# Kernel tuning notes

Hardware: AMD Instinct MI355X
Metric: run time of the kernel (lower is better)

The kernel has to match this reference:

```python
import jax, jax.numpy as jnp
import numpy as np

LMAX = 2
C = 128            # uniform multiplicity per degree
H = 128            # hidden channels
M = (LMAX + 1) ** 2  # 9 spherical coefficients
EPS = 1e-6


def _pack_indices():
    # flat layout per degree block: [mul, 2l+1] channel-major; packed layout: [coeff, channel]
    pack = np.zeros(M * C, dtype=np.int64)
    offset = 0
    for l in range(LMAX + 1):
        dim = 2 * l + 1
        for m in range(dim):
            coeff = l * l + m
            for c in range(C):
                pack[coeff * C + c] = offset + c * dim + m
        offset += C * dim
    unpack = np.argsort(pack)
    return jnp.asarray(pack), jnp.asarray(unpack)

PACK_IDX, UNPACK_IDX = _pack_indices()
# expand_index: degree index for each of the M coefficients
EXPAND_IDX = jnp.asarray(np.repeat(np.arange(LMAX + 1), 2 * np.arange(LMAX + 1) + 1))


def setup_inputs() -> dict:
    key = jax.random.key(0)
    ks = jax.random.split(key, 6)
    N = 10000
    A = 42  # (2*(lmax+1)) * (2*(lmax+1)+1) = 6*7 flattened S2 grid points
    bound = 1.0 / np.sqrt(C)
    return {
        "x": jax.random.normal(ks[0], (N, M * C), dtype=jnp.float32),
        "norm_weight": jnp.ones((LMAX + 1, C), dtype=jnp.float32),
        "w1": jax.random.uniform(ks[1], (LMAX + 1, H, C), jnp.float32, -bound, bound),
        "b1": jnp.zeros((1, 1, H), dtype=jnp.float32),
        "grid_w": jax.random.uniform(ks[2], (2 * H, H), jnp.float32, -bound, bound),
        "grid_b": jnp.zeros((2 * H,), dtype=jnp.float32),
        "w2": jax.random.uniform(ks[3], (LMAX + 1, C, H), jnp.float32, -bound, bound),
        "b2": jnp.zeros((1, 1, C), dtype=jnp.float32),
        "to_grid_mat": jax.random.normal(ks[4], (A, M), dtype=jnp.float32) * 0.3,
        "from_grid_mat": jax.random.normal(ks[5], (M, A), dtype=jnp.float32) * 0.3,
    }


def reference(x, norm_weight, w1, b1, grid_w, grid_b, w2, b2, to_grid_mat, from_grid_mat):
    N = x.shape[0]
    # --- pack flat irreps -> [N, M, C] (pure permutation gather; no padding for uniform irreps)
    p = jnp.take(x, PACK_IDX, axis=1).reshape(N, M, C)
    # --- merged equivariant RMS norm over all (coeff, channel), per-degree-channel affine
    rms = jnp.sqrt(jnp.mean(p * p, axis=(1, 2), keepdims=True) + EPS)
    h = (p / rms) * norm_weight[EXPAND_IDX][None]  # [N, M, C]
    # --- SO3LinearFlat #1: per-degree dense C -> H, bias only on l=0 coeff
    h = jnp.einsum("nmc,mhc->nmh", h, w1[EXPAND_IDX])
    h = h.at[:, 0:1, :].add(b1)
    # --- to S2 grid: [N, M, H] -> [N, A, H]
    g = jnp.einsum("am,nmh->nah", to_grid_mat, h)
    # --- pointwise SwiGLU on grid: H -> 2H linear, silu gate
    z = jnp.einsum("nah,oh->nao", g, grid_w) + grid_b
    g = jax.nn.silu(z[..., :H]) * z[..., H:]
    # --- from S2 grid: [N, A, H] -> [N, M, H]
    h = jnp.einsum("ma,nah->nmh", from_grid_mat, g)
    # --- SO3LinearFlat #2: per-degree dense H -> C, bias only on l=0 coeff
    out = jnp.einsum("nmh,mch->nmc", h, w2[EXPAND_IDX])
    out = out.at[:, 0:1, :].add(b2)
    # --- unpack back to flat irreps layout
    return jnp.take(out.reshape(N, M * C), UNPACK_IDX, axis=1)
```

## Files before the change

kernel.cpp:

```cpp
#include <hip/hip_runtime.h>
#include <math.h>

typedef unsigned short u16;
typedef __attribute__((ext_vector_type(8))) short bf16x8;
typedef __attribute__((ext_vector_type(4))) float f32x4;
typedef __attribute__((ext_vector_type(16))) float f32x16;

constexpr int OFF_W1 = 0;
constexpr int OFF_W2 = 49152;
constexpr int OFF_GW = 98304;
constexpr int OFF_TG = 131072;
constexpr int OFF_FG = 132096;
constexpr int WS_ELEMS = 134144;

__device__ __forceinline__ u16 f2bf(float f) {
    unsigned u = __float_as_uint(f);
    u += 0x7FFFu + ((u >> 16) & 1u);
    return (u16)(u >> 16);
}

__global__ void prep_kernel(const float* __restrict__ w1, const float* __restrict__ gw,
                            const float* __restrict__ w2, const float* __restrict__ tg,
                            const float* __restrict__ fg, u16* __restrict__ wsb) {
    const int idx = blockIdx.x * blockDim.x + threadIdx.x;
    const int str = gridDim.x * blockDim.x;
    for (int i = idx; i < 49152; i += str) wsb[OFF_W1 + i] = f2bf(w1[i]);
    for (int i = idx; i < 49152; i += str) wsb[OFF_W2 + i] = f2bf(w2[i]);
    for (int i = idx; i < 32768; i += str) wsb[OFF_GW + i] = f2bf(gw[i]);
    for (int i = idx; i < 1024; i += str) {
        int a = i >> 4, k = i & 15;
        wsb[OFF_TG + i] = (a < 42 && k < 9) ? f2bf(tg[a * 9 + k]) : (u16)0;
    }
    for (int i = idx; i < 2048; i += str) {
        int m = i >> 6, k = i & 63;
        wsb[OFF_FG + i] = (m < 9 && k < 42) ? f2bf(fg[m * 42 + k]) : (u16)0;
    }
}

__global__ __launch_bounds__(256, 2) void eqffn_mfma(
    const float* __restrict__ x, const float* __restrict__ nw,
    const float* __restrict__ b1f, const float* __restrict__ gbf,
    const float* __restrict__ b2f, const u16* __restrict__ wsb,
    float* __restrict__ out, int N)
{
    __shared__ u16 sh_a1[64 * 136];
    __shared__ u16 sh_h1T[4 * 128 * 16];
    __shared__ u16 sh_g[48 * 136];
    __shared__ u16 sh_g2T[128 * 72];
    __shared__ float sh_nw[384];
    __shared__ float sh_b1[128];
    __shared__ float sh_b2[128];
    __shared__ float sh_gb[256];

    const int tid  = threadIdx.x;
    const int w    = tid >> 6;
    const int lane = tid & 63;
    const int q    = lane >> 4;
    const int r    = lane & 15;
    const int r32  = lane & 31;
    const int half = lane >> 5;
    const int n0   = blockIdx.x * 4;

    for (int i = tid; i < 384; i += 256) sh_nw[i] = nw[i];
    if (tid < 128) { sh_b1[tid] = b1f[tid]; sh_b2[tid] = b2f[tid]; }
    sh_gb[tid] = gbf[tid];
    {
        unsigned long long* z1 = (unsigned long long*)sh_h1T;
        for (int i = tid; i < 2048; i += 256) z1[i] = 0ull;
        unsigned long long* z2 = (unsigned long long*)sh_g2T;
        for (int i = tid; i < 2304; i += 256) z2[i] = 0ull;
    }
    __syncthreads();

    const int myn = n0 + w;
    float4 xv[5];
    float ss = 0.f;
    if (myn < N) {
        const float4* xr = (const float4*)(x + (size_t)myn * 1152);
        for (int i = lane, c2 = 0; i < 288; i += 64, ++c2) {
            float4 v = xr[i]; xv[c2] = v;
            ss += v.x * v.x + v.y * v.y + v.z * v.z + v.w * v.w;
        }
    }
    #pragma unroll
    for (int off = 32; off; off >>= 1) ss += __shfl_xor(ss, off);
    const float inv = 1.0f / sqrtf(ss * (1.0f / 1152.0f) + 1e-6f);
    if (myn < N) {
        for (int i = lane, c2 = 0; i < 288; i += 64, ++c2) {
            float4 v = xv[c2];
            #pragma unroll
            for (int e = 0; e < 4; ++e) {
                const int f = i * 4 + e;
                const float val = ((const float*)&v)[e] * inv;
                int row, c, l;
                if (f < 128)      { l = 0; c = f;            row = w; }
                else if (f < 512) { int t = f - 128; l = 1; c = t / 3; row = 16 + w * 3 + (t - c * 3); }
                else              { int t = f - 512; l = 2; c = t / 5; row = 32 + w * 5 + (t - c * 5); }
                sh_a1[row * 136 + c] = f2bf(val * sh_nw[l * 128 + c]);
            }
        }
    }
    __syncthreads();

    {
        f32x4 acc[4][2];
        #pragma unroll
        for (int a = 0; a < 4; ++a)
            #pragma unroll
            for (int b = 0; b < 2; ++b)
                #pragma unroll
                for (int e = 0; e < 4; ++e) acc[a][b][e] = 0.f;
        #pragma unroll
        for (int mt = 0; mt < 4; ++mt) {
            const int l = (mt == 0) ? 0 : ((mt == 1) ? 1 : 2);
            #pragma unroll
            for (int k = 0; k < 4; ++k) {
                bf16x8 af = *(const bf16x8*)&sh_a1[(mt * 16 + r) * 136 + k * 32 + q * 8];
                #pragma unroll
                for (int nt = 0; nt < 2; ++nt) {
                    const int h = (2 * w + nt) * 16 + r;
                    bf16x8 bf = *(const bf16x8*)&wsb[OFF_W1 + (l * 128 + h) * 128 + k * 32 + q * 8];
                    acc[mt][nt] = __builtin_amdgcn_mfma_f32_16x16x32_bf16(af, bf, acc[mt][nt], 0, 0, 0);
                }
            }
        }
        #pragma unroll
        for (int mt = 0; mt < 4; ++mt) {
            #pragma unroll
            for (int nt = 0; nt < 2; ++nt) {
                const int h = (2 * w + nt) * 16 + r;
                #pragma unroll
                for (int rg = 0; rg < 4; ++rg) {
                    const int rr = q * 4 + rg;
                    const float v = acc[mt][nt][rg];
                    if (mt == 0) {
                        if (rr < 4) sh_h1T[(rr * 128 + h) * 16 + 0] = f2bf(v + sh_b1[h]);
                    } else if (mt == 1) {
                        if (rr < 12) { int nd = rr / 3, mm = rr - nd * 3; sh_h1T[(nd * 128 + h) * 16 + 1 + mm] = f2bf(v); }
                    } else {
                        int rr2 = (mt - 2) * 16 + rr;
                        if (rr2 < 20) { int nd = rr2 / 5, mm = rr2 - nd * 5; sh_h1T[(nd * 128 + h) * 16 + 4 + mm] = f2bf(v); }
                    }
                }
            }
        }
    }
    __syncthreads();

    for (int nn = 0; nn < 4; ++nn) {
        {
            bf16x8 bfr = *(const bf16x8*)&sh_h1T[(nn * 128 + w * 32 + r32) * 16 + half * 8];
            bf16x8 a0  = *(const bf16x8*)&wsb[OFF_TG + r32 * 16 + half * 8];
            bf16x8 a1  = *(const bf16x8*)&wsb[OFF_TG + (32 + r32) * 16 + half * 8];
            f32x16 ac0, ac1;
            #pragma unroll
            for (int e = 0; e < 16; ++e) { ac0[e] = 0.f; ac1[e] = 0.f; }
            ac0 = __builtin_amdgcn_mfma_f32_32x32x16_bf16(a0, bfr, ac0, 0, 0, 0);
            ac1 = __builtin_amdgcn_mfma_f32_32x32x16_bf16(a1, bfr, ac1, 0, 0, 0);
            const int h = w * 32 + r32;
            #pragma unroll
            for (int rg = 0; rg < 16; ++rg) {
                const int ar = (rg & 3) + 8 * (rg >> 2) + 4 * half;
                sh_g[ar * 136 + h] = f2bf(ac0[rg]);
                const int ar1 = 32 + ar;
                if (ar1 < 48) sh_g[ar1 * 136 + h] = f2bf(ac1[rg]);
            }
        }
        __syncthreads();

        {
            bf16x8 bfr[3][4];
            #pragma unroll
            for (int nt = 0; nt < 3; ++nt)
                #pragma unroll
                for (int k = 0; k < 4; ++k)
                    bfr[nt][k] = *(const bf16x8*)&sh_g[(nt * 16 + r) * 136 + k * 32 + q * 8];
            f32x4 aL[2][3], aH[2][3];
            #pragma unroll
            for (int p = 0; p < 2; ++p)
                #pragma unroll
                for (int nt = 0; nt < 3; ++nt)
                    #pragma unroll
                    for (int e = 0; e < 4; ++e) { aL[p][nt][e] = 0.f; aH[p][nt][e] = 0.f; }
            #pragma unroll
            for (int p = 0; p < 2; ++p) {
                const int oL = (2 * w + p) * 16 + r;
                const int oH = oL + 128;
                #pragma unroll
                for (int k = 0; k < 4; ++k) {
                    bf16x8 fL = *(const bf16x8*)&wsb[OFF_GW + oL * 128 + k * 32 + q * 8];
                    bf16x8 fH = *(const bf16x8*)&wsb[OFF_GW + oH * 128 + k * 32 + q * 8];
                    #pragma unroll
                    for (int nt = 0; nt < 3; ++nt) {
                        aL[p][nt] = __builtin_amdgcn_mfma_f32_16x16x32_bf16(fL, bfr[nt][k], aL[p][nt], 0, 0, 0);
                        aH[p][nt] = __builtin_amdgcn_mfma_f32_16x16x32_bf16(fH, bfr[nt][k], aH[p][nt], 0, 0, 0);
                    }
                }
            }
            #pragma unroll
            for (int p = 0; p < 2; ++p) {
                #pragma unroll
                for (int nt = 0; nt < 3; ++nt) {
                    #pragma unroll
                    for (int rg = 0; rg < 4; ++rg) {
                        const int o = (2 * w + p) * 16 + q * 4 + rg;
                        const int a = nt * 16 + r;
                        const float zl = aL[p][nt][rg] + sh_gb[o];
                        const float zh = aH[p][nt][rg] + sh_gb[128 + o];
                        const float gv = zl * (1.0f / (1.0f + __expf(-zl))) * zh;
                        if (a < 42) sh_g2T[o * 72 + a] = f2bf(gv);
                    }
                }
            }
        }
        __syncthreads();

        {
            f32x16 ac;
            #pragma unroll
            for (int e = 0; e < 16; ++e) ac[e] = 0.f;
            const int h = w * 32 + r32;
            #pragma unroll
            for (int k = 0; k < 4; ++k) {
                bf16x8 af = *(const bf16x8*)&wsb[OFF_FG + r32 * 64 + k * 16 + half * 8];
                bf16x8 bf = *(const bf16x8*)&sh_g2T[h * 72 + k * 16 + half * 8];
                ac = __builtin_amdgcn_mfma_f32_32x32x16_bf16(af, bf, ac, 0, 0, 0);
            }
            #pragma unroll
            for (int rg = 0; rg < 16; ++rg) {
                const int m = (rg & 3) + 8 * (rg >> 2) + 4 * half;
                if (m < 9) {
                    const int row = (m == 0) ? nn : ((m < 4) ? (16 + nn * 3 + (m - 1)) : (32 + nn * 5 + (m - 4)));
                    sh_a1[row * 136 + h] = f2bf(ac[rg]);
                }
            }
        }
    }
    __syncthreads();

    {
        f32x4 acc[4][2];
        #pragma unroll
        for (int a = 0; a < 4; ++a)
            #pragma unroll
            for (int b = 0; b < 2; ++b)
                #pragma unroll
                for (int e = 0; e < 4; ++e) acc[a][b][e] = 0.f;
        #pragma unroll
        for (int mt = 0; mt < 4; ++mt) {
            const int l = (mt == 0) ? 0 : ((mt == 1) ? 1 : 2);
            #pragma unroll
            for (int k = 0; k < 4; ++k) {
                bf16x8 af = *(const bf16x8*)&sh_a1[(mt * 16 + r) * 136 + k * 32 + q * 8];
                #pragma unroll
                for (int nt = 0; nt < 2; ++nt) {
                    const int c = (2 * w + nt) * 16 + r;
                    bf16x8 bf = *(const bf16x8*)&wsb[OFF_W2 + (l * 128 + c) * 128 + k * 32 + q * 8];
                    acc[mt][nt] = __builtin_amdgcn_mfma_f32_16x16x32_bf16(af, bf, acc[mt][nt], 0, 0, 0);
                }
            }
        }
        #pragma unroll
        for (int mt = 0; mt < 4; ++mt) {
            #pragma unroll
            for (int nt = 0; nt < 2; ++nt) {
                const int c = (2 * w + nt) * 16 + r;
                #pragma unroll
                for (int rg = 0; rg < 4; ++rg) {
                    const int rr = q * 4 + rg;
                    const float v = acc[mt][nt][rg];
                    if (mt == 0) {
                        if (rr < 4) { int gn = n0 + rr; if (gn < N) out[(size_t)gn * 1152 + c] = v + sh_b2[c]; }
                    } else if (mt == 1) {
                        if (rr < 12) { int nd = rr / 3, mm = rr - nd * 3; int gn = n0 + nd;
                                       if (gn < N) out[(size_t)gn * 1152 + 128 + c * 3 + mm] = v; }
                    } else {
                        int rr2 = (mt - 2) * 16 + rr;
                        if (rr2 < 20) { int nd = rr2 / 5, mm = rr2 - nd * 5; int gn = n0 + nd;
                                        if (gn < N) out[(size_t)gn * 1152 + 512 + c * 5 + mm] = v; }
                    }
                }
            }
        }
    }
}

extern "C" void kernel_launch(void* const* d_in, const int* in_sizes, int n_in,
                              void* d_out, int out_size, void* d_ws, size_t ws_size,
                              hipStream_t stream)
{
    const float* x  = (const float*)d_in[0];
    const float* nw = (const float*)d_in[1];
    const float* w1 = (const float*)d_in[2];
    const float* b1 = (const float*)d_in[3];
    const float* gw = (const float*)d_in[4];
    const float* gb = (const float*)d_in[5];
    const float* w2 = (const float*)d_in[6];
    const float* b2 = (const float*)d_in[7];
    const float* tg = (const float*)d_in[8];
    const float* fg = (const float*)d_in[9];
    float* out = (float*)d_out;
    u16* wsb = (u16*)d_ws;

    const int N = in_sizes[0] / 1152;
    prep_kernel<<<64, 256, 0, stream>>>(w1, gw, w2, tg, fg, wsb);
    eqffn_mfma<<<(N + 3) / 4, 256, 0, stream>>>(x, nw, b1, gb, b2, wsb, out, N);
}
```

Baseline: 257.2 us.

## Hoist grid-weight fragments into registers, trim from-grid K padding, relax barriers

Loads the to-grid, from-grid and grid_w MFMA operand fragments into registers once per block, instead of re-reading them from global memory on every one of the four per-node iterations. Shrinks the from-grid K padding from 64 to 48, so that stage needs three MFMAs instead of four. Pads the h1T LDS stride from 16 to 24. Restructures the barriers: sh_g is copied into registers before the barrier, and the barrier before the from-grid stage is dropped because each wave only reads the sh_g2T rows it wrote itself. The cost is many more live VGPRs, which risks spills or lower occupancy under the 256x2 launch bounds.

After: 257.1 us. Within noise of the previous version (-0.1%).

```diff
diff --git a/kernel.cpp b/kernel.cpp
--- a/kernel.cpp
+++ b/kernel.cpp
@@ -11,7 +11,7 @@
 constexpr int OFF_GW = 98304;
 constexpr int OFF_TG = 131072;
 constexpr int OFF_FG = 132096;
-constexpr int WS_ELEMS = 134144;
+constexpr int WS_ELEMS = 133632;
 
 __device__ __forceinline__ u16 f2bf(float f) {
     unsigned u = __float_as_uint(f);
@@ -31,8 +31,8 @@
         int a = i >> 4, k = i & 15;
         wsb[OFF_TG + i] = (a < 42 && k < 9) ? f2bf(tg[a * 9 + k]) : (u16)0;
     }
-    for (int i = idx; i < 2048; i += str) {
-        int m = i >> 6, k = i & 63;
+    for (int i = idx; i < 1536; i += str) {
+        int m = i / 48, k = i - m * 48;
         wsb[OFF_FG + i] = (m < 9 && k < 42) ? f2bf(fg[m * 42 + k]) : (u16)0;
     }
 }
@@ -44,9 +44,9 @@
     float* __restrict__ out, int N)
 {
     __shared__ u16 sh_a1[64 * 136];
-    __shared__ u16 sh_h1T[4 * 128 * 16];
+    __shared__ u16 sh_h1T[4 * 128 * 24];
     __shared__ u16 sh_g[48 * 136];
-    __shared__ u16 sh_g2T[128 * 72];
+    __shared__ u16 sh_g2T[128 * 56];
     __shared__ float sh_nw[384];
     __shared__ float sh_b1[128];
     __shared__ float sh_b2[128];
@@ -61,14 +61,31 @@
     const int half = lane >> 5;
     const int n0   = blockIdx.x * 4;
 
+    const bf16x8 tgA0 = *(const bf16x8*)&wsb[OFF_TG + r32 * 16 + half * 8];
+    const bf16x8 tgA1 = *(const bf16x8*)&wsb[OFF_TG + (32 + r32) * 16 + half * 8];
+    bf16x8 fgA[3];
+    #pragma unroll
+    for (int k = 0; k < 3; ++k)
+        fgA[k] = *(const bf16x8*)&wsb[OFF_FG + r32 * 48 + k * 16 + half * 8];
+    bf16x8 gwL[2][4], gwH[2][4];
+    #pragma unroll
+    for (int p = 0; p < 2; ++p) {
+        const int oL = (2 * w + p) * 16 + r;
+        #pragma unroll
+        for (int k = 0; k < 4; ++k) {
+            gwL[p][k] = *(const bf16x8*)&wsb[OFF_GW + oL * 128 + k * 32 + q * 8];
+            gwH[p][k] = *(const bf16x8*)&wsb[OFF_GW + (oL + 128) * 128 + k * 32 + q * 8];
+        }
+    }
+
     for (int i = tid; i < 384; i += 256) sh_nw[i] = nw[i];
     if (tid < 128) { sh_b1[tid] = b1f[tid]; sh_b2[tid] = b2f[tid]; }
     sh_gb[tid] = gbf[tid];
     {
         unsigned long long* z1 = (unsigned long long*)sh_h1T;
-        for (int i = tid; i < 2048; i += 256) z1[i] = 0ull;
+        for (int i = tid; i < 3072; i += 256) z1[i] = 0ull;
         unsigned long long* z2 = (unsigned long long*)sh_g2T;
-        for (int i = tid; i < 2304; i += 256) z2[i] = 0ull;
+        for (int i = tid; i < 1792; i += 256) z2[i] = 0ull;
     }
     __syncthreads();
 
@@ -134,12 +151,12 @@
                     const int rr = q * 4 + rg;
                     const float v = acc[mt][nt][rg];
                     if (mt == 0) {
-                        if (rr < 4) sh_h1T[(rr * 128 + h) * 16 + 0] = f2bf(v + sh_b1[h]);
+                        if (rr < 4) sh_h1T[(rr * 128 + h) * 24 + 0] = f2bf(v + sh_b1[h]);
                     } else if (mt == 1) {
-                        if (rr < 12) { int nd = rr / 3, mm = rr - nd * 3; sh_h1T[(nd * 128 + h) * 16 + 1 + mm] = f2bf(v); }
+                        if (rr < 12) { int nd = rr / 3, mm = rr - nd * 3; sh_h1T[(nd * 128 + h) * 24 + 1 + mm] = f2bf(v); }
                     } else {
                         int rr2 = (mt - 2) * 16 + rr;
-                        if (rr2 < 20) { int nd = rr2 / 5, mm = rr2 - nd * 5; sh_h1T[(nd * 128 + h) * 16 + 4 + mm] = f2bf(v); }
+                        if (rr2 < 20) { int nd = rr2 / 5, mm = rr2 - nd * 5; sh_h1T[(nd * 128 + h) * 24 + 4 + mm] = f2bf(v); }
                     }
                 }
             }
@@ -149,14 +166,12 @@
 
     for (int nn = 0; nn < 4; ++nn) {
         {
-            bf16x8 bfr = *(const bf16x8*)&sh_h1T[(nn * 128 + w * 32 + r32) * 16 + half * 8];
-            bf16x8 a0  = *(const bf16x8*)&wsb[OFF_TG + r32 * 16 + half * 8];
-            bf16x8 a1  = *(const bf16x8*)&wsb[OFF_TG + (32 + r32) * 16 + half * 8];
+            bf16x8 bfn = *(const bf16x8*)&sh_h1T[(nn * 128 + w * 32 + r32) * 24 + half * 8];
             f32x16 ac0, ac1;
             #pragma unroll
             for (int e = 0; e < 16; ++e) { ac0[e] = 0.f; ac1[e] = 0.f; }
-            ac0 = __builtin_amdgcn_mfma_f32_32x32x16_bf16(a0, bfr, ac0, 0, 0, 0);
-            ac1 = __builtin_amdgcn_mfma_f32_32x32x16_bf16(a1, bfr, ac1, 0, 0, 0);
+            ac0 = __builtin_amdgcn_mfma_f32_32x32x16_bf16(tgA0, bfn, ac0, 0, 0, 0);
+            ac1 = __builtin_amdgcn_mfma_f32_32x32x16_bf16(tgA1, bfn, ac1, 0, 0, 0);
             const int h = w * 32 + r32;
             #pragma unroll
             for (int rg = 0; rg < 16; ++rg) {
@@ -168,52 +183,47 @@
         }
         __syncthreads();
 
-        {
-            bf16x8 bfr[3][4];
+        bf16x8 bfr[3][4];
+        #pragma unroll
+        for (int nt = 0; nt < 3; ++nt)
+            #pragma unroll
+            for (int k = 0; k < 4; ++k)
+                bfr[nt][k] = *(const bf16x8*)&sh_g[(nt * 16 + r) * 136 + k * 32 + q * 8];
+        __syncthreads();
+
+        f32x4 aL[2][3], aH[2][3];
+        #pragma unroll
+        for (int p = 0; p < 2; ++p)
             #pragma unroll
             for (int nt = 0; nt < 3; ++nt)
                 #pragma unroll
-                for (int k = 0; k < 4; ++k)
-                    bfr[nt][k] = *(const bf16x8*)&sh_g[(nt * 16 + r) * 136 + k * 32 + q * 8];
-            f32x4 aL[2][3], aH[2][3];
-            #pragma unroll
-            for (int p = 0; p < 2; ++p)
-                #pragma unroll
-                for (int nt = 0; nt < 3; ++nt)
-                    #pragma unroll
-                    for (int e = 0; e < 4; ++e) { aL[p][nt][e] = 0.f; aH[p][nt][e] = 0.f; }
-            #pragma unroll
-            for (int p = 0; p < 2; ++p) {
-                const int oL = (2 * w + p) * 16 + r;
-                const int oH = oL + 128;
-                #pragma unroll
-                for (int k = 0; k < 4; ++k) {
-                    bf16x8 fL = *(const bf16x8*)&wsb[OFF_GW + oL * 128 + k * 32 + q * 8];
-                    bf16x8 fH = *(const bf16x8*)&wsb[OFF_GW + oH * 128 + k * 32 + q * 8];
-                    #pragma unroll
-                    for (int nt = 0; nt < 3; ++nt) {
-                        aL[p][nt] = __builtin_amdgcn_mfma_f32_16x16x32_bf16(fL, bfr[nt][k], aL[p][nt], 0, 0, 0);
-                        aH[p][nt] = __builtin_amdgcn_mfma_f32_16x16x32_bf16(fH, bfr[nt][k], aH[p][nt], 0, 0, 0);
-                    }
-                }
-            }
-            #pragma unroll
-            for (int p = 0; p < 2; ++p) {
+                for (int e = 0; e < 4; ++e) { aL[p][nt][e] = 0.f; aH[p][nt][e] = 0.f; }
+        #pragma unroll
+        for (int p = 0; p < 2; ++p) {
+            #pragma unroll
+            for (int k = 0; k < 4; ++k) {
                 #pragma unroll
                 for (int nt = 0; nt < 3; ++nt) {
-                    #pragma unroll
-                    for (int rg = 0; rg < 4; ++rg) {
-                        const int o = (2 * w + p) * 16 + q * 4 + rg;
-                        const int a = nt * 16 + r;
-                        const float zl = aL[p][nt][rg] + sh_gb[o];
-                        const float zh = aH[p][nt][rg] + sh_gb[128 + o];
-                        const float gv = zl * (1.0f / (1.0f + __expf(-zl))) * zh;
-                        if (a < 42) sh_g2T[o * 72 + a] = f2bf(gv);
-                    }
-                }
-            }
-        }
-        __syncthreads();
+                    aL[p][nt] = __builtin_amdgcn_mfma_f32_16x16x32_bf16(gwL[p][k], bfr[nt][k], aL[p][nt], 0, 0, 0);
+                    aH[p][nt] = __builtin_amdgcn_mfma_f32_16x16x32_bf16(gwH[p][k], bfr[nt][k], aH[p][nt], 0, 0, 0);
+                }
+            }
+        }
+        #pragma unroll
+        for (int p = 0; p < 2; ++p) {
+            #pragma unroll
+            for (int nt = 0; nt < 3; ++nt) {
+                #pragma unroll
+                for (int rg = 0; rg < 4; ++rg) {
+                    const int o = (2 * w + p) * 16 + q * 4 + rg;
+                    const int a = nt * 16 + r;
+                    const float zl = aL[p][nt][rg] + sh_gb[o];
+                    const float zh = aH[p][nt][rg] + sh_gb[128 + o];
+                    const float gv = zl * (1.0f / (1.0f + __expf(-zl))) * zh;
+                    if (a < 42) sh_g2T[o * 56 + a] = f2bf(gv);
+                }
+            }
+        }
 
         {
             f32x16 ac;
@@ -221,10 +231,9 @@
             for (int e = 0; e < 16; ++e) ac[e] = 0.f;
             const int h = w * 32 + r32;
             #pragma unroll
-            for (int k = 0; k < 4; ++k) {
-                bf16x8 af = *(const bf16x8*)&wsb[OFF_FG + r32 * 64 + k * 16 + half * 8];
-                bf16x8 bf = *(const bf16x8*)&sh_g2T[h * 72 + k * 16 + half * 8];
-                ac = __builtin_amdgcn_mfma_f32_32x32x16_bf16(af, bf, ac, 0, 0, 0);
+            for (int k = 0; k < 3; ++k) {
+                bf16x8 bv = *(const bf16x8*)&sh_g2T[h * 56 + k * 16 + half * 8];
+                ac = __builtin_amdgcn_mfma_f32_32x32x16_bf16(fgA[k], bv, ac, 0, 0, 0);
             }
             #pragma unroll
             for (int rg = 0; rg < 16; ++rg) {
```
